# Kernel tuning notes

Hardware: AMD Instinct MI355X
Metric: run time of the kernel (lower is better)

Reference implementation:

```python
import jax, jax.numpy as jnp
import numpy as np


def setup_inputs() -> dict:
    key = jax.random.key(0)
    ks = jax.random.split(key, 7)
    B, T, I, H, O = 256, 1024, 3, 128, 3
    s = 1.0 / np.sqrt(H)  # torch nn.RNN/Linear default init scale
    return {
        "inputs": jax.random.normal(ks[0], (B, T, I), dtype=jnp.float32),
        "W_ih": jax.random.uniform(ks[1], (H, I), jnp.float32, -s, s),
        "W_hh": jax.random.uniform(ks[2], (H, H), jnp.float32, -s, s),
        "b_ih": jax.random.uniform(ks[3], (H,), jnp.float32, -s, s),
        "b_hh": jax.random.uniform(ks[4], (H,), jnp.float32, -s, s),
        "h0": jnp.zeros((1, H), dtype=jnp.float32),  # learned initial hidden (init zeros)
        "W_out": jax.random.uniform(ks[5], (O, H), jnp.float32, -s, s),
        "b_out": jax.random.uniform(ks[6], (O,), jnp.float32, -s, s),
    }


def reference(inputs, W_ih, W_hh, b_ih, b_hh, h0, W_out, b_out):
    # inputs: [B, T, I]; Elman RNN with tanh, batch_first, single layer.
    B = inputs.shape[0]
    # Precompute input projection for all timesteps: [T, B, H]
    x_proj = jnp.einsum('bti,hi->tbh', inputs, W_ih) + b_ih + b_hh
    h_init = jnp.broadcast_to(h0, (B, h0.shape[1]))

    def step(h, xp):
        h_new = jnp.tanh(xp + h @ W_hh.T)
        return h_new, h_new

    _, hiddens_tbh = jax.lax.scan(step, h_init, x_proj)
    hiddens = jnp.transpose(hiddens_tbh, (1, 0, 2))  # [B, T, H]
    output = jnp.einsum('bth,oh->bto', hiddens, W_out) + b_out  # [B, T, O]
    return output, hiddens
```

## Files before the change

kernel.cpp:

```cpp
#include <hip/hip_runtime.h>

#define BB 256
#define TT 1024
#define II 3
#define HH 128
#define OO 3
#define NT 576

#if __has_builtin(__builtin_amdgcn_exp2f)
#define EXP2F __builtin_amdgcn_exp2f
#else
#define EXP2F exp2f
#endif
#if __has_builtin(__builtin_amdgcn_rcpf)
#define RCPF __builtin_amdgcn_rcpf
#else
#define RCPF(x) (1.0f / (x))
#endif

__device__ __forceinline__ float fast_tanh(float x) {
    float e = EXP2F(x * 2.885390081777927f);
    return 1.0f - 2.0f * RCPF(e + 1.0f);
}

__device__ __forceinline__ void bar_lds() {
    asm volatile("s_waitcnt lgkmcnt(0)\n\ts_barrier" ::: "memory");
}

__global__ __launch_bounds__(NT) void rnn_kernel(
    const float* __restrict__ x,
    const float* __restrict__ Wih,
    const float* __restrict__ Whh,
    const float* __restrict__ bih,
    const float* __restrict__ bhh,
    const float* __restrict__ h0,
    const float* __restrict__ Wout,
    const float* __restrict__ bout,
    float* __restrict__ out,
    float* __restrict__ hid)
{
    __shared__ __align__(16) float4 xs[TT];
    __shared__ __align__(16) float hbuf[2][HH];

    const int tid = threadIdx.x;
    const int b = blockIdx.x;

    const float* xb = x + (size_t)b * TT * II;
    for (int idx = tid; idx < TT * II; idx += NT) {
        int t = idx / 3;
        int c = idx - t * 3;
        ((float*)&xs[t])[c] = xb[idx];
    }
    if (tid < HH) hbuf[0][tid] = h0[tid];

    if (tid < 512) {
        const int lane = tid & 63;
        const int wv   = tid >> 6;
        const int o16  = lane & 15;
        const int sub  = lane >> 4;
        const int h    = wv * 16 + o16;

        float w[32];
        {
            const float4* wp = (const float4*)(Whh + h * HH + 32 * sub);
#pragma unroll
            for (int j = 0; j < 8; j++) {
                float4 v = wp[j];
                w[4 * j + 0] = v.x;
                w[4 * j + 1] = v.y;
                w[4 * j + 2] = v.z;
                w[4 * j + 3] = v.w;
            }
        }
        const float wi0 = Wih[h * II + 0];
        const float wi1 = Wih[h * II + 1];
        const float wi2 = Wih[h * II + 2];
        const float bias = bih[h] + bhh[h];

        bar_lds();

        for (int t = 0; t < TT; t++) {
            const float* hcur = hbuf[t & 1];
            float* hnext = hbuf[(t + 1) & 1];

            float a0 = 0.f, a1 = 0.f, a2 = 0.f, a3 = 0.f;
            if (sub == 0) {
                float4 xv = xs[t];
                a0 = fmaf(xv.x, wi0, bias);
                a0 = fmaf(xv.y, wi1, a0);
                a0 = fmaf(xv.z, wi2, a0);
            }
            const float4* hv = (const float4*)(hcur + 32 * sub);
#pragma unroll
            for (int j = 0; j < 8; j++) {
                float4 hh = hv[j];
                a0 = fmaf(w[4 * j + 0], hh.x, a0);
                a1 = fmaf(w[4 * j + 1], hh.y, a1);
                a2 = fmaf(w[4 * j + 2], hh.z, a2);
                a3 = fmaf(w[4 * j + 3], hh.w, a3);
            }
            float s = (a0 + a1) + (a2 + a3);
            s += __shfl_xor(s, 16);
            s += __shfl_xor(s, 32);
            float th = fast_tanh(s);
            if (sub == 0) hnext[h] = th;
            bar_lds();
        }
    } else {
        const int L = tid - 512;
        const float w00 = Wout[0 * HH + 2 * L], w01 = Wout[0 * HH + 2 * L + 1];
        const float w10 = Wout[1 * HH + 2 * L], w11 = Wout[1 * HH + 2 * L + 1];
        const float w20 = Wout[2 * HH + 2 * L], w21 = Wout[2 * HH + 2 * L + 1];
        const float b0 = bout[0], b1 = bout[1], b2 = bout[2];
        float* ob = out + (size_t)b * TT * OO;
        float* hb = hid + (size_t)b * TT * HH;

        bar_lds();

        for (int t = 0; t < TT; t++) {
            if (t > 0) {
                const float2 hv = ((const float2*)hbuf[t & 1])[L];
                ((float2*)(hb + (size_t)(t - 1) * HH))[L] = hv;
                float p0 = fmaf(hv.x, w00, hv.y * w01);
                float p1 = fmaf(hv.x, w10, hv.y * w11);
                float p2 = fmaf(hv.x, w20, hv.y * w21);
#pragma unroll
                for (int m = 32; m >= 1; m >>= 1) {
                    p0 += __shfl_xor(p0, m);
                    p1 += __shfl_xor(p1, m);
                    p2 += __shfl_xor(p2, m);
                }
                if (L == 0) {
                    float* o = ob + (size_t)(t - 1) * OO;
                    o[0] = p0 + b0;
                    o[1] = p1 + b1;
                    o[2] = p2 + b2;
                }
            }
            bar_lds();
        }
        {
            const float2 hv = ((const float2*)hbuf[0])[L];
            ((float2*)(hb + (size_t)(TT - 1) * HH))[L] = hv;
            float p0 = fmaf(hv.x, w00, hv.y * w01);
            float p1 = fmaf(hv.x, w10, hv.y * w11);
            float p2 = fmaf(hv.x, w20, hv.y * w21);
#pragma unroll
            for (int m = 32; m >= 1; m >>= 1) {
                p0 += __shfl_xor(p0, m);
                p1 += __shfl_xor(p1, m);
                p2 += __shfl_xor(p2, m);
            }
            if (L == 0) {
                float* o = ob + (size_t)(TT - 1) * OO;
                o[0] = p0 + b0;
                o[1] = p1 + b1;
                o[2] = p2 + b2;
            }
        }
    }
}

extern "C" void kernel_launch(void* const* d_in, const int* in_sizes, int n_in,
                              void* d_out, int out_size, void* d_ws, size_t ws_size,
                              hipStream_t stream) {
    const float* x    = (const float*)d_in[0];
    const float* Wih  = (const float*)d_in[1];
    const float* Whh  = (const float*)d_in[2];
    const float* bih  = (const float*)d_in[3];
    const float* bhh  = (const float*)d_in[4];
    const float* h0   = (const float*)d_in[5];
    const float* Wout = (const float*)d_in[6];
    const float* bout = (const float*)d_in[7];

    float* out = (float*)d_out;
    float* hid = out + (size_t)BB * TT * OO;

    rnn_kernel<<<BB, NT, 0, stream>>>(x, Wih, Whh, bih, bhh, h0, Wout, bout, out, hid);
}
```

Baseline: 542.6 us.

## Batch 8 sequences per block and run recurrence on bf16x3 MFMA

Each block now handles 8 batch rows instead of one, and the hidden-state matmul per step runs on 16x16x32 bf16 MFMA. A split hi/lo bf16 (three-product) scheme keeps the result close to fp32 accuracy. Work is split across warp roles: input projection into a double-buffered LDS, the recurrence, the hidden-state store, and the output projection with DPP reductions. LDS layouts are XOR-swizzled. The grid shrinks from 256 to 32 blocks, so far fewer CUs are busy, and the recurrence now pays MFMA latency on every one of the 1024 serial steps.

```diff
diff --git a/kernel.cpp b/kernel.cpp
--- a/kernel.cpp
+++ b/kernel.cpp
@@ -5,7 +5,14 @@
 #define II 3
 #define HH 128
 #define OO 3
-#define NT 576
+#define BT 8
+#define NBLK (BB / BT)
+#define NT 512
+
+typedef __attribute__((ext_vector_type(8))) short short8;
+typedef __attribute__((ext_vector_type(4))) float f32x4;
+typedef __attribute__((ext_vector_type(4))) unsigned int uint4v;
+typedef __attribute__((ext_vector_type(2))) unsigned int uint2v;
 
 #if __has_builtin(__builtin_amdgcn_exp2f)
 #define EXP2F __builtin_amdgcn_exp2f
@@ -26,6 +33,31 @@
 __device__ __forceinline__ void bar_lds() {
     asm volatile("s_waitcnt lgkmcnt(0)\n\ts_barrier" ::: "memory");
 }
+
+template <int CTRL>
+__device__ __forceinline__ float dpp_add(float p) {
+    return p + __uint_as_float(__builtin_amdgcn_update_dpp(
+        0, (int)__float_as_uint(p), CTRL, 0xF, 0xF, true));
+}
+#define DPP_XOR1 0xB1
+#define DPP_XOR2 0x4E
+#define DPP_HALF_MIRROR 0x141
+
+__device__ __forceinline__ unsigned int bf16pk(float a, float b) {
+    unsigned int r;
+    asm("v_cvt_pk_bf16_f32 %0, %1, %2" : "=v"(r) : "v"(a), "v"(b));
+    return r;
+}
+__device__ __forceinline__ float f_lo16(unsigned int p) { return __uint_as_float(p << 16); }
+__device__ __forceinline__ float f_hi16(unsigned int p) { return __uint_as_float(p & 0xffff0000u); }
+
+__device__ __forceinline__ f32x4 MFMA(uint4v a, uint4v b, f32x4 c) {
+    return __builtin_amdgcn_mfma_f32_16x16x32_bf16(
+        __builtin_bit_cast(short8, a), __builtin_bit_cast(short8, b), c, 0, 0, 0);
+}
+
+__device__ __forceinline__ int swzH(int bb, int k) { return (((k >> 3) ^ bb) << 3) | (k & 7); }
+__device__ __forceinline__ int swzF(int bb, int k) { return (((k >> 2) ^ bb) << 2) | (k & 3); }
 
 __global__ __launch_bounds__(NT) void rnn_kernel(
     const float* __restrict__ x,
@@ -39,125 +71,255 @@
     float* __restrict__ out,
     float* __restrict__ hid)
 {
-    __shared__ __align__(16) float4 xs[TT];
-    __shared__ __align__(16) float hbuf[2][HH];
+    __shared__ __align__(16) float4 xs[TT][BT];
+    __shared__ __align__(16) ushort Hhi[2][BT][HH];
+    __shared__ __align__(16) ushort Hlo[2][BT][HH];
+    __shared__ __align__(16) float  H32[2][BT][HH];
+    __shared__ __align__(16) float  XP[2][BT][HH];
 
     const int tid = threadIdx.x;
-    const int b = blockIdx.x;
-
-    const float* xb = x + (size_t)b * TT * II;
-    for (int idx = tid; idx < TT * II; idx += NT) {
-        int t = idx / 3;
-        int c = idx - t * 3;
-        ((float*)&xs[t])[c] = xb[idx];
+    const int b0 = blockIdx.x * BT;
+
+    const float* xb = x + (size_t)b0 * TT * II;
+    for (int idx = tid; idx < BT * TT * II; idx += NT) {
+        int bb = idx / (TT * II);
+        int r = idx - bb * (TT * II);
+        int t = r / II;
+        int c = r - t * II;
+        ((float*)&xs[t][bb])[c] = xb[idx];
     }
-    if (tid < HH) hbuf[0][tid] = h0[tid];
-
-    if (tid < 512) {
-        const int lane = tid & 63;
-        const int wv   = tid >> 6;
-        const int o16  = lane & 15;
-        const int sub  = lane >> 4;
-        const int h    = wv * 16 + o16;
-
-        float w[32];
+    for (int idx = tid; idx < BT * HH; idx += NT) {
+        int bb = idx >> 7, h = idx & (HH - 1);
+        float v = h0[h];
+        unsigned int p = bf16pk(v, 0.f);
+        float vh = f_lo16(p);
+        unsigned int q = bf16pk(v - vh, 0.f);
+        Hhi[0][bb][swzH(bb, h)] = (ushort)(p & 0xffffu);
+        Hlo[0][bb][swzH(bb, h)] = (ushort)(q & 0xffffu);
+        H32[0][bb][swzF(bb, h)] = v;
+    }
+    __syncthreads();
+
+    const int wv = tid >> 6;
+    const int lane = tid & 63;
+
+    if (wv < 4) {
+        const int col = lane & 15;
+        const int act = col < BT;
+        const int colc = act ? col : (BT - 1);
+        const int kb = (lane >> 4) * 8;
+        const int r0 = wv * 32 + (lane >> 4) * 4;
+
+        uint4v Ahi[2][4], Alo[2][4];
+#pragma unroll
+        for (int tau = 0; tau < 2; ++tau) {
+            const int row = wv * 32 + tau * 16 + col;
+            const float* wrow = Whh + row * HH + kb;
+#pragma unroll
+            for (int c = 0; c < 4; ++c) {
+                float4 wa = *(const float4*)(wrow + c * 32);
+                float4 wb = *(const float4*)(wrow + c * 32 + 4);
+                unsigned int h01 = bf16pk(wa.x, wa.y), h23 = bf16pk(wa.z, wa.w);
+                unsigned int h45 = bf16pk(wb.x, wb.y), h67 = bf16pk(wb.z, wb.w);
+                unsigned int l01 = bf16pk(wa.x - f_lo16(h01), wa.y - f_hi16(h01));
+                unsigned int l23 = bf16pk(wa.z - f_lo16(h23), wa.w - f_hi16(h23));
+                unsigned int l45 = bf16pk(wb.x - f_lo16(h45), wb.y - f_hi16(h45));
+                unsigned int l67 = bf16pk(wb.z - f_lo16(h67), wb.w - f_hi16(h67));
+                Ahi[tau][c] = uint4v{h01, h23, h45, h67};
+                Alo[tau][c] = uint4v{l01, l23, l45, l67};
+            }
+        }
+
+        int rdB[4], wrHi0, wrHi1, rdX0, rdX1, wrF0, wrF1;
+#pragma unroll
+        for (int c = 0; c < 4; ++c) rdB[c] = ((c * 4 + (kb >> 3)) ^ colc) << 3;
+        wrHi0 = swzH(colc, r0);
+        wrHi1 = swzH(colc, r0 + 16);
+        rdX0 = swzF(colc, r0);
+        rdX1 = swzF(colc, r0 + 16);
+        wrF0 = rdX0;
+        wrF1 = rdX1;
+
+        uint4v bh[4] = {}, bl[4] = {};
+        f32x4 xp0 = {0.f, 0.f, 0.f, 0.f}, xp1 = {0.f, 0.f, 0.f, 0.f};
+
+        bar_lds();
+
+        auto cwin = [&](const ushort* bhiP, const ushort* bloP, const float* xpP,
+                        ushort* ohiP, ushort* oloP, float* o32P) {
+            if (act) {
+#pragma unroll
+                for (int c = 0; c < 4; ++c) {
+                    bh[c] = *(const uint4v*)(bhiP + rdB[c]);
+                    bl[c] = *(const uint4v*)(bloP + rdB[c]);
+                }
+                xp0 = *(const f32x4*)(xpP + rdX0);
+                xp1 = *(const f32x4*)(xpP + rdX1);
+            }
+            f32x4 a0 = xp0, a1 = {0.f, 0.f, 0.f, 0.f}, a2 = {0.f, 0.f, 0.f, 0.f};
+            f32x4 c0 = xp1, c1 = {0.f, 0.f, 0.f, 0.f}, c2 = {0.f, 0.f, 0.f, 0.f};
+#pragma unroll
+            for (int c = 0; c < 4; ++c) {
+                a0 = MFMA(Ahi[0][c], bh[c], a0);
+                a1 = MFMA(Ahi[0][c], bl[c], a1);
+                a2 = MFMA(Alo[0][c], bh[c], a2);
+                c0 = MFMA(Ahi[1][c], bh[c], c0);
+                c1 = MFMA(Ahi[1][c], bl[c], c1);
+                c2 = MFMA(Alo[1][c], bh[c], c2);
+            }
+            f32x4 s0 = (a0 + a1) + a2;
+            f32x4 s1 = (c0 + c1) + c2;
+            float t0 = fast_tanh(s0.x), t1 = fast_tanh(s0.y);
+            float t2 = fast_tanh(s0.z), t3 = fast_tanh(s0.w);
+            float u0 = fast_tanh(s1.x), u1 = fast_tanh(s1.y);
+            float u2 = fast_tanh(s1.z), u3 = fast_tanh(s1.w);
+            if (act) {
+                unsigned int p0 = bf16pk(t0, t1), p1 = bf16pk(t2, t3);
+                unsigned int q0 = bf16pk(t0 - f_lo16(p0), t1 - f_hi16(p0));
+                unsigned int q1 = bf16pk(t2 - f_lo16(p1), t3 - f_hi16(p1));
+                *(uint2v*)(ohiP + wrHi0) = uint2v{p0, p1};
+                *(uint2v*)(oloP + wrHi0) = uint2v{q0, q1};
+                *(f32x4*)(o32P + wrF0) = f32x4{t0, t1, t2, t3};
+                unsigned int p2 = bf16pk(u0, u1), p3 = bf16pk(u2, u3);
+                unsigned int q2 = bf16pk(u0 - f_lo16(p2), u1 - f_hi16(p2));
+                unsigned int q3 = bf16pk(u2 - f_lo16(p3), u3 - f_hi16(p3));
+                *(uint2v*)(ohiP + wrHi1) = uint2v{p2, p3};
+                *(uint2v*)(oloP + wrHi1) = uint2v{q2, q3};
+                *(f32x4*)(o32P + wrF1) = f32x4{u0, u1, u2, u3};
+            }
+            bar_lds();
+        };
+
+        for (int t = 0; t < TT; t += 2) {
+            cwin(&Hhi[0][colc][0], &Hlo[0][colc][0], &XP[0][colc][0],
+                 &Hhi[1][colc][0], &Hlo[1][colc][0], &H32[1][colc][0]);
+            cwin(&Hhi[1][colc][0], &Hlo[1][colc][0], &XP[1][colc][0],
+                 &Hhi[0][colc][0], &Hlo[0][colc][0], &H32[0][colc][0]);
+        }
+    } else if (wv < 6) {
+        const int h = (wv - 4) * 64 + lane;
+        const float wi0 = Wih[h * II + 0], wi1 = Wih[h * II + 1], wi2 = Wih[h * II + 2];
+        const float bias = bih[h] + bhh[h];
+        const int hs = (h & 3);
+        const int hc = h >> 2;
+
+#pragma unroll
+        for (int bb = 0; bb < BT; ++bb) {
+            float4 xv = xs[0][bb];
+            float v = fmaf(xv.z, wi2, fmaf(xv.y, wi1, fmaf(xv.x, wi0, bias)));
+            XP[0][bb][((hc ^ bb) << 2) | hs] = v;
+        }
+        bar_lds();
+
+        for (int t = 0; t < TT; t += 2) {
+            {
+#pragma unroll
+                for (int bb = 0; bb < BT; ++bb) {
+                    float4 xv = xs[t + 1][bb];
+                    float v = fmaf(xv.z, wi2, fmaf(xv.y, wi1, fmaf(xv.x, wi0, bias)));
+                    XP[1][bb][((hc ^ bb) << 2) | hs] = v;
+                }
+                bar_lds();
+            }
+            {
+                if (t + 2 < TT) {
+#pragma unroll
+                    for (int bb = 0; bb < BT; ++bb) {
+                        float4 xv = xs[t + 2][bb];
+                        float v = fmaf(xv.z, wi2, fmaf(xv.y, wi1, fmaf(xv.x, wi0, bias)));
+                        XP[0][bb][((hc ^ bb) << 2) | hs] = v;
+                    }
+                }
+                bar_lds();
+            }
+        }
+    } else if (wv == 6) {
+        const int bb = lane >> 3;
+        const int hh0 = (lane & 7) * 16;
+        float* hb = hid + ((size_t)(b0 + bb) * TT) * HH + hh0;
+        const float* s0p = &H32[0][bb][0];
+        const float* s1p = &H32[1][bb][0];
+        int off[4];
+#pragma unroll
+        for (int c = 0; c < 4; ++c) off[c] = ((((lane & 7) * 4 + c) ^ bb) << 2);
+
+        bar_lds();
+        for (int t = 0; t < TT; t += 2) {
+            if (t > 0) {
+                float* g = hb + (size_t)(t - 1) * HH;
+#pragma unroll
+                for (int c = 0; c < 4; ++c)
+                    *(f32x4*)(g + c * 4) = *(const f32x4*)(s0p + off[c]);
+            }
+            bar_lds();
+            {
+                float* g = hb + (size_t)t * HH;
+#pragma unroll
+                for (int c = 0; c < 4; ++c)
+                    *(f32x4*)(g + c * 4) = *(const f32x4*)(s1p + off[c]);
+            }
+            bar_lds();
+        }
         {
-            const float4* wp = (const float4*)(Whh + h * HH + 32 * sub);
-#pragma unroll
-            for (int j = 0; j < 8; j++) {
-                float4 v = wp[j];
-                w[4 * j + 0] = v.x;
-                w[4 * j + 1] = v.y;
-                w[4 * j + 2] = v.z;
-                w[4 * j + 3] = v.w;
-            }
-        }
-        const float wi0 = Wih[h * II + 0];
-        const float wi1 = Wih[h * II + 1];
-        const float wi2 = Wih[h * II + 2];
-        const float bias = bih[h] + bhh[h];
+            float* g = hb + (size_t)(TT - 1) * HH;
+#pragma unroll
+            for (int c = 0; c < 4; ++c)
+                *(f32x4*)(g + c * 4) = *(const f32x4*)(s0p + off[c]);
+        }
+    } else {
+        const int bb = lane >> 3;
+        const int ks = lane & 7;
+        float w[3][16];
+#pragma unroll
+        for (int o = 0; o < 3; ++o)
+#pragma unroll
+            for (int j = 0; j < 4; ++j) {
+                float4 v = *(const float4*)(Wout + o * HH + ks * 16 + j * 4);
+                w[o][j * 4 + 0] = v.x;
+                w[o][j * 4 + 1] = v.y;
+                w[o][j * 4 + 2] = v.z;
+                w[o][j * 4 + 3] = v.w;
+            }
+        const float bo0 = bout[0], bo1 = bout[1], bo2 = bout[2];
+        float* ob = out + (size_t)(b0 + bb) * TT * OO;
+        const float* s0p = &H32[0][bb][0];
+        const float* s1p = &H32[1][bb][0];
+        int off[4];
+#pragma unroll
+        for (int c = 0; c < 4; ++c) off[c] = (((ks * 4 + c) ^ bb) << 2);
+
+        auto proj = [&](const float* sp, float* op) {
+            f32x4 u[4];
+#pragma unroll
+            for (int c = 0; c < 4; ++c) u[c] = *(const f32x4*)(sp + off[c]);
+            float p0 = 0.f, p1 = 0.f, p2 = 0.f;
+#pragma unroll
+            for (int c = 0; c < 4; ++c) {
+                p0 = fmaf(w[0][c * 4 + 0], u[c].x, p0); p0 = fmaf(w[0][c * 4 + 1], u[c].y, p0);
+                p0 = fmaf(w[0][c * 4 + 2], u[c].z, p0); p0 = fmaf(w[0][c * 4 + 3], u[c].w, p0);
+                p1 = fmaf(w[1][c * 4 + 0], u[c].x, p1); p1 = fmaf(w[1][c * 4 + 1], u[c].y, p1);
+                p1 = fmaf(w[1][c * 4 + 2], u[c].z, p1); p1 = fmaf(w[1][c * 4 + 3], u[c].w, p1);
+                p2 = fmaf(w[2][c * 4 + 0], u[c].x, p2); p2 = fmaf(w[2][c * 4 + 1], u[c].y, p2);
+                p2 = fmaf(w[2][c * 4 + 2], u[c].z, p2); p2 = fmaf(w[2][c * 4 + 3], u[c].w, p2);
+            }
+            p0 = dpp_add<DPP_XOR1>(p0); p0 = dpp_add<DPP_XOR2>(p0); p0 = dpp_add<DPP_HALF_MIRROR>(p0);
+            p1 = dpp_add<DPP_XOR1>(p1); p1 = dpp_add<DPP_XOR2>(p1); p1 = dpp_add<DPP_HALF_MIRROR>(p1);
+            p2 = dpp_add<DPP_XOR1>(p2); p2 = dpp_add<DPP_XOR2>(p2); p2 = dpp_add<DPP_HALF_MIRROR>(p2);
+            if (ks == 0) {
+                op[0] = p0 + bo0;
+                op[1] = p1 + bo1;
+                op[2] = p2 + bo2;
+            }
+        };
 
         bar_lds();
-
-        for (int t = 0; t < TT; t++) {
-            const float* hcur = hbuf[t & 1];
-            float* hnext = hbuf[(t + 1) & 1];
-
-            float a0 = 0.f, a1 = 0.f, a2 = 0.f, a3 = 0.f;
-            if (sub == 0) {
-                float4 xv = xs[t];
-                a0 = fmaf(xv.x, wi0, bias);
-                a0 = fmaf(xv.y, wi1, a0);
-                a0 = fmaf(xv.z, wi2, a0);
-            }
-            const float4* hv = (const float4*)(hcur + 32 * sub);
-#pragma unroll
-            for (int j = 0; j < 8; j++) {
-                float4 hh = hv[j];
-                a0 = fmaf(w[4 * j + 0], hh.x, a0);
-                a1 = fmaf(w[4 * j + 1], hh.y, a1);
-                a2 = fmaf(w[4 * j + 2], hh.z, a2);
-                a3 = fmaf(w[4 * j + 3], hh.w, a3);
-            }
-            float s = (a0 + a1) + (a2 + a3);
-            s += __shfl_xor(s, 16);
-            s += __shfl_xor(s, 32);
-            float th = fast_tanh(s);
-            if (sub == 0) hnext[h] = th;
-            bar_lds();
-        }
-    } else {
-        const int L = tid - 512;
-        const float w00 = Wout[0 * HH + 2 * L], w01 = Wout[0 * HH + 2 * L + 1];
-        const float w10 = Wout[1 * HH + 2 * L], w11 = Wout[1 * HH + 2 * L + 1];
-        const float w20 = Wout[2 * HH + 2 * L], w21 = Wout[2 * HH + 2 * L + 1];
-        const float b0 = bout[0], b1 = bout[1], b2 = bout[2];
-        float* ob = out + (size_t)b * TT * OO;
-        float* hb = hid + (size_t)b * TT * HH;
-
-        bar_lds();
-
-        for (int t = 0; t < TT; t++) {
-            if (t > 0) {
-                const float2 hv = ((const float2*)hbuf[t & 1])[L];
-                ((float2*)(hb + (size_t)(t - 1) * HH))[L] = hv;
-                float p0 = fmaf(hv.x, w00, hv.y * w01);
-                float p1 = fmaf(hv.x, w10, hv.y * w11);
-                float p2 = fmaf(hv.x, w20, hv.y * w21);
-#pragma unroll
-                for (int m = 32; m >= 1; m >>= 1) {
-                    p0 += __shfl_xor(p0, m);
-                    p1 += __shfl_xor(p1, m);
-                    p2 += __shfl_xor(p2, m);
-                }
-                if (L == 0) {
-                    float* o = ob + (size_t)(t - 1) * OO;
-                    o[0] = p0 + b0;
-                    o[1] = p1 + b1;
-                    o[2] = p2 + b2;
-                }
-            }
-            bar_lds();
-        }
-        {
-            const float2 hv = ((const float2*)hbuf[0])[L];
-            ((float2*)(hb + (size_t)(TT - 1) * HH))[L] = hv;
-            float p0 = fmaf(hv.x, w00, hv.y * w01);
-            float p1 = fmaf(hv.x, w10, hv.y * w11);
-            float p2 = fmaf(hv.x, w20, hv.y * w21);
-#pragma unroll
-            for (int m = 32; m >= 1; m >>= 1) {
-                p0 += __shfl_xor(p0, m);
-                p1 += __shfl_xor(p1, m);
-                p2 += __shfl_xor(p2, m);
-            }
-            if (L == 0) {
-                float* o = ob + (size_t)(TT - 1) * OO;
-                o[0] = p0 + b0;
-                o[1] = p1 + b1;
-                o[2] = p2 + b2;
-            }
-        }
+        for (int t = 0; t < TT; t += 2) {
+            if (t > 0) proj(s0p, ob + (size_t)(t - 1) * OO);
+            bar_lds();
+            proj(s1p, ob + (size_t)t * OO);
+            bar_lds();
+        }
+        proj(s0p, ob + (size_t)(TT - 1) * OO);
     }
 }
 
@@ -176,5 +338,5 @@
     float* out = (float*)d_out;
     float* hid = out + (size_t)BB * TT * OO;
 
-    rnn_kernel<<<BB, NT, 0, stream>>>(x, Wih, Whh, bih, bhh, h0, Wout, bout, out, hid);
-}
+    rnn_kernel<<<NBLK, NT, 0, stream>>>(x, Wih, Whh, bih, bhh, h0, Wout, bout, out, hid);
+}
```

Result: slower. 661.6 us (+21.9%).
